# Performance work log

Hardware: AMD Instinct MI355X
Metric: run time of the kernel (lower is better)

Reference implementation:

```python
import jax, jax.numpy as jnp
import numpy as np

T, B, E, H = 64, 64, 128, 256
N_ITEMS, N_DATA = 50000, 20000
EPS = 1e-8


def setup_inputs() -> dict:
    key = jax.random.key(0)
    ks = jax.random.split(key, 20)
    lengths = jnp.sort(jax.random.randint(ks[0], (B,), 1, T + 1))[::-1]
    lengths = lengths.at[0].set(T)  # pack_padded_sequence expects max length first
    x = jax.random.randint(ks[1], (T, B), 1, N_ITEMS)
    tmask = jnp.arange(T)[:, None] < lengths[None, :]
    x = jnp.where(tmask, x, 0)  # padding index 0
    s = 0.05
    emb_table = (jax.random.normal(ks[2], (N_ITEMS, E)) * s).at[0].set(0.0)  # padding_idx=0
    data_embeddings = jax.random.normal(ks[3], (N_DATA, E)) * s
    return {
        'x': x, 'lengths': lengths,
        'emb_table': emb_table, 'data_embeddings': data_embeddings,
        'W_ih': jax.random.normal(ks[4], (4 * H, E)) * s,
        'W_hh': jax.random.normal(ks[5], (4 * H, H)) * s,
        'b_ih': jax.random.normal(ks[6], (4 * H,)) * s,
        'b_hh': jax.random.normal(ks[7], (4 * H,)) * s,
        'Wq': jax.random.normal(ks[8], (H, H)) * s, 'bq': jax.random.normal(ks[9], (H,)) * s,
        'Wk': jax.random.normal(ks[10], (H, H)) * s, 'bk': jax.random.normal(ks[11], (H,)) * s,
        'Wv': jax.random.normal(ks[12], (H, H)) * s, 'bv': jax.random.normal(ks[13], (H,)) * s,
        'W_out': jax.random.normal(ks[14], (E, H)) * s, 'b_out': jax.random.normal(ks[15], (E,)) * s,
    }


def _forward(x, lengths, emb_table, data_embeddings, W_ih, W_hh, b_ih, b_hh,
             Wq, bq, Wk, bk, Wv, bv, W_out, b_out):
    t_len, b_sz = x.shape
    e_dim = emb_table.shape[1]
    h_dim = W_hh.shape[1]

    embs0 = emb_table[x]  # (T, B, E); dropout is identity in eval mode
    initial_embs = jax.lax.stop_gradient(embs0)  # .clone().detach() in original

    # PositionalEncoding: original slices by x.size(1) == batch dim (faithful quirk)
    pos = jnp.arange(b_sz, dtype=jnp.float32)[:, None]
    div = jnp.exp(jnp.arange(0, e_dim, 2, dtype=jnp.float32) * (-jnp.log(10000.0) / e_dim))
    enc = jnp.stack([jnp.sin(pos * div), jnp.cos(pos * div)], axis=-1).reshape(b_sz, e_dim)
    embs = embs0 + enc[None, :, :]  # broadcast over time

    # single-layer LSTM over time (gate order i, f, g, o)
    def step(carry, x_t):
        h, c = carry
        gates = x_t @ W_ih.T + h @ W_hh.T + (b_ih + b_hh)  # (B, 4H)
        i, f, g, o = jnp.split(gates, 4, axis=-1)
        c = jax.nn.sigmoid(f) * c + jax.nn.sigmoid(i) * jnp.tanh(g)
        h = jax.nn.sigmoid(o) * jnp.tanh(c)
        return (h, c), h

    h0 = jnp.zeros((b_sz, h_dim), embs.dtype)
    (_, _), lstm_out = jax.lax.scan(step, (h0, h0), embs)  # (T, B, H)

    # pack/pad round-trip zeroes outputs past each length (LSTM is causal)
    tmask = jnp.arange(t_len)[:, None] < lengths[None, :]  # (T, B)
    lstm_out = lstm_out * tmask[:, :, None]
    lstm_out = lstm_out.transpose(1, 0, 2)  # (B, T, H)

    padding_mask = jnp.sum(lstm_out, axis=-1) != 0  # (B, T)

    q = lstm_out @ Wq.T + bq
    k = lstm_out @ Wk.T + bk
    v = lstm_out @ Wv.T + bv
    score = jnp.einsum('bth,bsh->bts', q, k) / jnp.sqrt(jnp.float32(h_dim))
    score = jnp.where(padding_mask[:, None, :], score, -jnp.inf)
    attn = jax.nn.softmax(score, axis=2)
    weighted = jnp.einsum('bts,bsh->bth', attn, v)  # (B, T, H)
    attn_output = jnp.mean(weighted, axis=1) @ W_out.T + b_out  # (B, E)

    # kNN: fused normalize + matmul + argmin + gather over all T at once
    qn = initial_embs / jnp.clip(jnp.linalg.norm(initial_embs, axis=-1, keepdims=True), EPS)
    dn = data_embeddings / jnp.clip(jnp.linalg.norm(data_embeddings, axis=-1, keepdims=True), EPS)
    sims = jnp.einsum('tbe,ne->tbn', qn, dn)  # (T, B, N_DATA)
    idx = jnp.argmax(sims, axis=-1)  # argmin of (1 - sim)
    closest = jnp.mean(data_embeddings[idx], axis=0)  # (B, E)

    attn_output = attn_output * closest
    return attn_output @ emb_table.T  # (B, n_items)


def reference(x, lengths, emb_table, data_embeddings, W_ih, W_hh, b_ih, b_hh,
              Wq, bq, Wk, bk, Wv, bv, W_out, b_out):
    return _forward(x, lengths, emb_table, data_embeddings, W_ih, W_hh, b_ih, b_hh,
                    Wq, bq, Wk, bk, Wv, bv, W_out, b_out)
```

## Files before the change

kernel.cpp:

```cpp
#include <hip/hip_runtime.h>

typedef unsigned int uint;
typedef unsigned short ushort;
typedef unsigned long long u64;

#define NITEMS 50000
#define NDATA  20000
#define BLKCAP 4096u
#define OVCAP  65536u

#define OFF_LSTMOUT   0x0000000ULL
#define OFF_HX        0x0400000ULL
#define OFF_PACKED    0x0440000ULL
#define OFF_PACKED2   0x0448000ULL
#define OFF_HITCNTS   0x0450000ULL
#define OFF_OHITCNT   0x0450800ULL
#define MEMSET_BYTES  0x0451000ULL
#define OFF_QMARGIN   0x0451000ULL
#define OFF_XW        0x0560000ULL
#define OFF_QKV       0x1560000ULL
#define OFF_HITBUF    OFF_QKV
#define OFF_WIHT      0x2160000ULL
#define OFF_WQKVT     0x21E0000ULL
#define OFF_BIASIH    0x22A0000ULL
#define OFF_BQKV      0x22A1000ULL
#define OFF_DNSCALE   0x22A2000ULL
#define OFF_CLOSEST   0x22B6000ULL
#define OFF_AV        0x22BE000ULL
#define OFF_DEMB16    0x22C6000ULL
#define OFF_A16       0x27A8000ULL

__device__ __forceinline__ ushort f2bf(float f) {
  union { float f; uint u; } v; v.f = f;
  uint u = v.u;
  return (ushort)((u + 0x7FFFu + ((u >> 16) & 1u)) >> 16);
}
__device__ __forceinline__ uint fkey(float f) {
  union { float f; uint u; } v; v.f = f;
  return (v.u & 0x80000000u) ? ~v.u : (v.u | 0x80000000u);
}
__device__ __forceinline__ u64 shfl_xor_u64(u64 v, int off) {
  uint lo = (uint)v, hi = (uint)(v >> 32);
  lo = (uint)__shfl_xor((int)lo, off);
  hi = (uint)__shfl_xor((int)hi, off);
  return ((u64)hi << 32) | (u64)lo;
}

typedef __attribute__((ext_vector_type(8))) short short8;
typedef __attribute__((ext_vector_type(4))) float floatx4;

#define R32(M) M(0) M(1) M(2) M(3) M(4) M(5) M(6) M(7) M(8) M(9) M(10) M(11) \
  M(12) M(13) M(14) M(15) M(16) M(17) M(18) M(19) M(20) M(21) M(22) M(23) \
  M(24) M(25) M(26) M(27) M(28) M(29) M(30) M(31)

__global__ __launch_bounds__(256) void prep_kernel(
    const int* __restrict__ x,
    const float* __restrict__ emb, const float* __restrict__ demb,
    const float* __restrict__ W_ih,
    const float* __restrict__ Wq, const float* __restrict__ Wk, const float* __restrict__ Wv,
    const float* __restrict__ b_ih, const float* __restrict__ b_hh,
    const float* __restrict__ bq, const float* __restrict__ bk, const float* __restrict__ bv,
    float* __restrict__ dnscale, ushort* __restrict__ demb16, ushort* __restrict__ a16,
    float* __restrict__ wiht, float* __restrict__ wqkvt,
    float* __restrict__ biasih, float* __restrict__ bqkv,
    float* __restrict__ qmargin, u64* __restrict__ packed2)
{
  int blk = blockIdx.x, tid = threadIdx.x;
  if (blk < 5000) {
    int row = blk * 4 + (tid >> 6);
    int lane = tid & 63;
    float2 d = *(const float2*)(demb + (size_t)row * 128 + lane * 2);
    float s = d.x * d.x + d.y * d.y;
    for (int off = 32; off; off >>= 1) s += __shfl_xor(s, off);
    if (lane == 0) dnscale[row] = 1.0f / fmaxf(sqrtf(s), 1e-8f);
  } else if (blk < 6250) {
    size_t base = ((size_t)(blk - 5000) * 256 + tid) * 8;
    float4 f1 = *(const float4*)(demb + base);
    float4 f2 = *(const float4*)(demb + base + 4);
    uint4 o;
    o.x = (uint)f2bf(f1.x) | ((uint)f2bf(f1.y) << 16);
    o.y = (uint)f2bf(f1.z) | ((uint)f2bf(f1.w) << 16);
    o.z = (uint)f2bf(f2.x) | ((uint)f2bf(f2.y) << 16);
    o.w = (uint)f2bf(f2.z) | ((uint)f2bf(f2.w) << 16);
    *(uint4*)(demb16 + base) = o;
  } else if (blk < 6506) {
    int idx = (blk - 6250) * 256 + tid;
    int m = idx >> 4, seg = idx & 15;
    const float* src = emb + (size_t)x[m] * 128 + seg * 8;
    float4 f1 = *(const float4*)(src);
    float4 f2 = *(const float4*)(src + 4);
    uint4 o;
    o.x = (uint)f2bf(f1.x) | ((uint)f2bf(f1.y) << 16);
    o.y = (uint)f2bf(f1.z) | ((uint)f2bf(f1.w) << 16);
    o.z = (uint)f2bf(f2.x) | ((uint)f2bf(f2.y) << 16);
    o.w = (uint)f2bf(f2.z) | ((uint)f2bf(f2.w) << 16);
    *(uint4*)(a16 + (size_t)m * 128 + seg * 8) = o;
  } else if (blk < 7018) {
    int f = (blk - 6506) * 256 + tid;
    int r = f >> 7, e = f & 127;
    wiht[e * 1024 + r] = W_ih[f];
  } else if (blk < 7786) {
    int f = (blk - 7018) * 256 + tid;
    int w = f >> 16; int rem = f & 65535;
    int r = rem >> 8, e = rem & 255;
    const float* src = (w == 0) ? Wq : (w == 1) ? Wk : Wv;
    wqkvt[e * 768 + w * 256 + r] = src[rem];
  } else if (blk < 7790) {
    int idx = (blk - 7786) * 256 + tid;
    if (idx < 1024) biasih[idx] = b_ih[idx] + b_hh[idx];
  } else if (blk < 7793) {
    int idx = (blk - 7790) * 256 + tid;
    if (idx < 768) {
      int w = idx >> 8; int r = idx & 255;
      const float* src = (w == 0) ? bq : (w == 1) ? bk : bv;
      bqkv[idx] = src[r];
    }
  } else {
    int row = (blk - 7793) * 4 + (tid >> 6);
    int lane = tid & 63;
    float2 d = *(const float2*)(emb + (size_t)x[row] * 128 + lane * 2);
    float s = d.x * d.x + d.y * d.y;
    for (int off = 32; off; off >>= 1) s += __shfl_xor(s, off);
    if (lane == 0) {
      if (s == 0.f) {
        qmargin[row] = -1e30f;
        packed2[row] = ((u64)fkey(0.0f) << 32) | 0xFFFFFFFFull;
      } else {
        qmargin[row] = 0.017f * sqrtf(s) + 1e-5f;
      }
    }
  }
}

__global__ __launch_bounds__(256) void xw_kernel(
    const int* __restrict__ x, const float* __restrict__ emb,
    const float* __restrict__ wiht, const float* __restrict__ biasih,
    float* __restrict__ xW)
{
  __shared__ __align__(16) float At[128 * 16];
  int blk = blockIdx.x, tid = threadIdx.x;
  int m0 = blk * 16;
  for (int c = 0; c < 8; ++c) {
    int idx = c * 256 + tid;
    int mm = idx >> 7, e = idx & 127;
    int m = m0 + mm;
    int bcol = m & 63;
    int xv = x[m];
    float val = emb[(size_t)xv * 128 + e];
    int j = e >> 1;
    float arg = (float)bcol * __expf((float)j * -0.14391157f);
    val += (e & 1) ? cosf(arg) : sinf(arg);
    At[e * 16 + mm] = val;
  }
  __syncthreads();
  int quad = tid >> 6, l = tid & 63;
  for (int rp = 0; rp < 4; ++rp) {
    int r = rp * 256 + l * 4;
    float acc[4][4] = {};
    for (int e = 0; e < 128; ++e) {
      float4 wv4 = *(const float4*)(wiht + e * 1024 + r);
      float4 av4 = *(const float4*)(At + e * 16 + quad * 4);
      float am[4] = {av4.x, av4.y, av4.z, av4.w};
      float wr4[4] = {wv4.x, wv4.y, wv4.z, wv4.w};
      #pragma unroll
      for (int mi = 0; mi < 4; ++mi)
        #pragma unroll
        for (int ri = 0; ri < 4; ++ri)
          acc[mi][ri] += am[mi] * wr4[ri];
    }
    float4 bv4 = *(const float4*)(biasih + r);
    #pragma unroll
    for (int mi = 0; mi < 4; ++mi) {
      size_t m = (size_t)(m0 + quad * 4 + mi);
      float4 o;
      o.x = acc[mi][0] + bv4.x; o.y = acc[mi][1] + bv4.y;
      o.z = acc[mi][2] + bv4.z; o.w = acc[mi][3] + bv4.w;
      *(float4*)(xW + m * 1024 + r) = o;
    }
  }
}

__global__ __launch_bounds__(256) void knn_kernel(
    const ushort* __restrict__ a16, const ushort* __restrict__ demb16,
    const float* __restrict__ dnscale, const float* __restrict__ qmargin,
    u64* __restrict__ packed, uint* __restrict__ hitcnts, uint* __restrict__ ohitcnt,
    uint* __restrict__ hitbuf)
{
  __shared__ __align__(16) ushort b_sh[2][64 * 144];
  __shared__ uint lcnt;
  int blk = blockIdx.x, tid = threadIdx.x;
  int chunk = blk & 15, mt = blk >> 4;
  int wv = tid >> 6, lane = tid & 63;
  int col = lane & 15, quad = lane >> 4;
  int M0 = mt * 128;
  if (tid == 0) lcnt = 0;
  short8 afrag[2][4];
  #pragma unroll
  for (int s = 0; s < 2; ++s) {
    int mrow = M0 + s * 64 + wv * 16 + col;
    #pragma unroll
    for (int kf = 0; kf < 4; ++kf)
      afrag[s][kf] = *(const short8*)(a16 + (size_t)mrow * 128 + kf * 32 + quad * 8);
  }
  float best[2][4] = {{-1e30f,-1e30f,-1e30f,-1e30f},{-1e30f,-1e30f,-1e30f,-1e30f}};
  int bidx[2][4] = {};
  int nbase = chunk * 1250, nend = nbase + 1250;
  const int niter = 20;
  int srow = tid >> 4, sseg = tid & 15;
  uint4 stg[4]; float scr[4];

  #pragma unroll
  for (int p = 0; p < 4; ++p) {
    int n = nbase + p * 16 + srow;
    uint4 v = {0u,0u,0u,0u};
    if (n < nend) v = *(const uint4*)(demb16 + (size_t)n * 128 + sseg * 8);
    stg[p] = v;
  }
  #pragma unroll
  for (int ns = 0; ns < 4; ++ns) {
    int n = nbase + ns * 16 + col;
    scr[ns] = (n < nend) ? dnscale[n] : 0.f;
  }
  for (int it = 0; it < niter; ++it) {
    int n0 = nbase + it * 64;
    ushort* bsh = b_sh[it & 1];
    #pragma unroll
    for (int p = 0; p < 4; ++p)
      *(uint4*)(&bsh[(p * 16 + srow) * 144 + sseg * 8]) = stg[p];
    float mysc[4] = {scr[0], scr[1], scr[2], scr[3]};
    __syncthreads();
    if (it + 1 < niter) {
      int nb = n0 + 64;
      #pragma unroll
      for (int p = 0; p < 4; ++p) {
        int n = nb + p * 16 + srow;
        uint4 v = {0u,0u,0u,0u};
        if (n < nend) v = *(const uint4*)(demb16 + (size_t)n * 128 + sseg * 8);
        stg[p] = v;
      }
      #pragma unroll
      for (int ns = 0; ns < 4; ++ns) {
        int n = nb + ns * 16 + col;
        scr[ns] = (n < nend) ? dnscale[n] : 0.f;
      }
    }
    #pragma unroll
    for (int ns = 0; ns < 4; ++ns) {
      short8 bfr[4];
      #pragma unroll
      for (int kf = 0; kf < 4; ++kf)
        bfr[kf] = *(const short8*)(&bsh[(ns * 16 + col) * 144 + kf * 32 + quad * 8]);
      int n = n0 + ns * 16 + col;
      float sc = mysc[ns];
      bool valid = (n < nend);
      #pragma unroll
      for (int s = 0; s < 2; ++s) {
        floatx4 acc = {0.f, 0.f, 0.f, 0.f};
        #pragma unroll
        for (int kf = 0; kf < 4; ++kf)
          acc = __builtin_amdgcn_mfma_f32_16x16x32_bf16(afrag[s][kf], bfr[kf], acc, 0, 0, 0);
        #pragma unroll
        for (int r = 0; r < 4; ++r) {
          float sim = acc[r] * sc;
          if (valid && sim > best[s][r]) { best[s][r] = sim; bidx[s][r] = n; }
        }
      }
    }
  }
  float thr[2][4];
  #pragma unroll
  for (int s = 0; s < 2; ++s)
    #pragma unroll
    for (int r = 0; r < 4; ++r) {
      u64 p = ((u64)fkey(best[s][r]) << 32) | (u64)(0xFFFFFFFFu - (uint)bidx[s][r]);
      #pragma unroll
      for (int off = 1; off < 16; off <<= 1) {
        u64 o = shfl_xor_u64(p, off);
        if (o > p) p = o;
      }
      int m = M0 + s * 64 + wv * 16 + quad * 4 + r;
      union { uint u; float f; } bu;
      uint k = (uint)(p >> 32);
      bu.u = (k & 0x80000000u) ? (k & 0x7FFFFFFFu) : ~k;
      thr[s][r] = bu.f - qmargin[m];
      if (col == 0)
        atomicMax((unsigned long long*)&packed[m], (unsigned long long)p);
    }
  __syncthreads();

  uint* myregion = hitbuf + (size_t)blk * BLKCAP;
  uint* ovregion = hitbuf + (size_t)512 * BLKCAP;
  #pragma unroll
  for (int p = 0; p < 4; ++p) {
    int n = nbase + p * 16 + srow;
    uint4 v = {0u,0u,0u,0u};
    if (n < nend) v = *(const uint4*)(demb16 + (size_t)n * 128 + sseg * 8);
    stg[p] = v;
  }
  #pragma unroll
  for (int ns = 0; ns < 4; ++ns) {
    int n = nbase + ns * 16 + col;
    scr[ns] = (n < nend) ? dnscale[n] : 0.f;
  }
  for (int it = 0; it < niter; ++it) {
    int n0 = nbase + it * 64;
    ushort* bsh = b_sh[it & 1];
    #pragma unroll
    for (int p = 0; p < 4; ++p)
      *(uint4*)(&bsh[(p * 16 + srow) * 144 + sseg * 8]) = stg[p];
    float mysc[4] = {scr[0], scr[1], scr[2], scr[3]};
    __syncthreads();
    if (it + 1 < niter) {
      int nb = n0 + 64;
      #pragma unroll
      for (int p = 0; p < 4; ++p) {
        int n = nb + p * 16 + srow;
        uint4 v = {0u,0u,0u,0u};
        if (n < nend) v = *(const uint4*)(demb16 + (size_t)n * 128 + sseg * 8);
        stg[p] = v;
      }
      #pragma unroll
      for (int ns = 0; ns < 4; ++ns) {
        int n = nb + ns * 16 + col;
        scr[ns] = (n < nend) ? dnscale[n] : 0.f;
      }
    }
    #pragma unroll
    for (int ns = 0; ns < 4; ++ns) {
      short8 bfr[4];
      #pragma unroll
      for (int kf = 0; kf < 4; ++kf)
        bfr[kf] = *(const short8*)(&bsh[(ns * 16 + col) * 144 + kf * 32 + quad * 8]);
      int n = n0 + ns * 16 + col;
      float sc = mysc[ns];
      bool valid = (n < nend);
      #pragma unroll
      for (int s = 0; s < 2; ++s) {
        floatx4 acc = {0.f, 0.f, 0.f, 0.f};
        #pragma unroll
        for (int kf = 0; kf < 4; ++kf)
          acc = __builtin_amdgcn_mfma_f32_16x16x32_bf16(afrag[s][kf], bfr[kf], acc, 0, 0, 0);
        #pragma unroll
        for (int r = 0; r < 4; ++r) {
          float sim = acc[r] * sc;
          bool hit = valid && (sim >= thr[s][r]);
          u64 mask = __ballot(hit);
          if (mask) {
            uint lcntv = (uint)__popcll(mask);
            int leader = __ffsll((unsigned long long)mask) - 1;
            uint base = 0;
            if (lane == leader) base = atomicAdd(&lcnt, lcntv);
            base = (uint)__shfl((int)base, leader);
            if (hit) {
              uint pos = base + (uint)__popcll(mask & ((1ull << lane) - 1ull));
              uint mm = (uint)(M0 + s * 64 + wv * 16 + quad * 4 + r);
              uint rec = (mm << 15) | (uint)n;
              if (pos < BLKCAP) {
                myregion[pos] = rec;
              } else {
                uint op = atomicAdd(ohitcnt, 1u);
                if (op < OVCAP) ovregion[op] = rec;
              }
            }
          }
        }
      }
    }
  }
  __syncthreads();
  if (tid == 0) hitcnts[blk] = lcnt;
}

__global__ __launch_bounds__(256) void rescore_kernel(
    const uint* __restrict__ hitbuf, const uint* __restrict__ hitcnts,
    const uint* __restrict__ ohitcnt, const u64* __restrict__ packed,
    const int* __restrict__ x, const float* __restrict__ emb,
    const float* __restrict__ demb, const float* __restrict__ dnscale,
    u64* __restrict__ packed2)
{
  int blk = blockIdx.x, tid = threadIdx.x;
  uint gid = blk * 256 + tid;
  if (gid < 4096) {
    uint m = gid;
    uint n = 0xFFFFFFFFu - (uint)(packed[m] & 0xFFFFFFFFull);
    if (n < NDATA) {
      const float* q = emb + (size_t)x[m] * 128;
      const float* d = demb + (size_t)n * 128;
      double p = 0.0;
      #pragma unroll 8
      for (int e = 0; e < 128; e += 2) {
        float2 qv = *(const float2*)(q + e);
        float2 dv = *(const float2*)(d + e);
        p += (double)qv.x * (double)dv.x + (double)qv.y * (double)dv.y;
      }
      float sx = (float)(p * (double)dnscale[n]);
      u64 key = ((u64)fkey(sx) << 32) | (u64)(0xFFFFFFFFu - n);
      atomicMax((unsigned long long*)&packed2[m], (unsigned long long)key);
    }
  }
  const uint* src; uint cnt; uint stride;
  if (blk < 512) {
    src = hitbuf + (size_t)blk * BLKCAP;
    cnt = hitcnts[blk]; if (cnt > BLKCAP) cnt = BLKCAP;
    stride = 256;
  } else {
    src = hitbuf + (size_t)512 * BLKCAP + (blk - 512) * 256 + 0;
    src = hitbuf + (size_t)512 * BLKCAP;
    cnt = *ohitcnt; if (cnt > OVCAP) cnt = OVCAP;
    stride = 16 * 256;
  }
  uint start = (blk < 512) ? tid : (uint)((blk - 512) * 256 + tid);
  for (uint h = start; h < cnt; h += stride) {
    uint rec = src[h];
    uint m = rec >> 15, n = rec & 0x7FFFu;
    if (m >= 4096 || n >= NDATA) continue;
    const float* q = emb + (size_t)x[m] * 128;
    const float* d = demb + (size_t)n * 128;
    double p = 0.0;
    #pragma unroll 8
    for (int e = 0; e < 128; e += 2) {
      float2 qv = *(const float2*)(q + e);
      float2 dv = *(const float2*)(d + e);
      p += (double)qv.x * (double)dv.x + (double)qv.y * (double)dv.y;
    }
    float sx = (float)(p * (double)dnscale[n]);
    u64 key = ((u64)fkey(sx) << 32) | (u64)(0xFFFFFFFFu - n);
    atomicMax((unsigned long long*)&packed2[m], (unsigned long long)key);
  }
}

__global__ __launch_bounds__(512, 2) void lstm_kernel(
    const int* __restrict__ lengths, const float* __restrict__ Whh,
    const float* __restrict__ xW, float* __restrict__ lstm_out,
    u64* __restrict__ hx)
{
  __shared__ __align__(16) float h_sh[256];
  __shared__ float part_sh[512];
  int blk = blockIdx.x, tid = threadIdx.x;
  int b = blk & 63, q = blk >> 6;
  int row_local = tid >> 1, half = tid & 1;
  int gate = row_local >> 6, jloc = row_local & 63;
  int grow = gate * 256 + q * 64 + jloc;
  const float4* wp4 = (const float4*)(Whh + (size_t)grow * 256 + half * 128);
#define WDECL(i) float4 tt##i = wp4[i]; \
  float w##i##x = tt##i.x, w##i##y = tt##i.y, w##i##z = tt##i.z, w##i##w = tt##i.w;
  R32(WDECL)
#define WPIN(i) asm volatile("" : "+v"(w##i##x), "+v"(w##i##y), "+v"(w##i##z), "+v"(w##i##w));
  R32(WPIN)
  int len = lengths[b];
  if (tid < 256) h_sh[tid] = 0.f;
  float cval = 0.f;
  int jr = (tid < q * 64) ? tid : tid + 64;
  __syncthreads();
  for (int t = 0; t < len; ++t) {
    if (t > 0) {
      if (tid < 192) {
        u64* slot = hx + (((size_t)(t & 1) * 64 + b) * 256 + jr);
        u64 v = 0; int guard = 0;
        while (true) {
          v = __hip_atomic_load(slot, __ATOMIC_RELAXED, __HIP_MEMORY_SCOPE_AGENT);
          if ((uint)v == (uint)t || ++guard > (1 << 22)) break;
          __builtin_amdgcn_s_sleep(1);
        }
        union { uint u; float f; } cv; cv.u = (uint)(v >> 32);
        h_sh[jr] = cv.f;
      }
      __syncthreads();
    }
    const float4* h4 = (const float4*)(h_sh + half * 128);
    float acc = 0.f;
#define WACC(i) { float4 hv = h4[i]; \
    acc += w##i##x * hv.x + w##i##y * hv.y + w##i##z * hv.z + w##i##w * hv.w; }
    R32(WACC)
    part_sh[tid] = acc;
    __syncthreads();
    if (tid < 64) {
      const float* xwrow = xW + ((size_t)t * 64 + b) * 1024 + q * 64 + tid;
      float gi = part_sh[tid * 2]         + part_sh[tid * 2 + 1]         + xwrow[0];
      float gf = part_sh[(64 + tid) * 2]  + part_sh[(64 + tid) * 2 + 1]  + xwrow[256];
      float gg = part_sh[(128 + tid) * 2] + part_sh[(128 + tid) * 2 + 1] + xwrow[512];
      float go = part_sh[(192 + tid) * 2] + part_sh[(192 + tid) * 2 + 1] + xwrow[768];
      float ii = 1.f / (1.f + __expf(-gi));
      float ff = 1.f / (1.f + __expf(-gf));
      float oo = 1.f / (1.f + __expf(-go));
      cval = ff * cval + ii * tanhf(gg);
      float hv = oo * tanhf(cval);
      int j = q * 64 + tid;
      lstm_out[((size_t)b * 64 + t) * 256 + j] = hv;
      h_sh[j] = hv;
      union { float f; uint u; } cu; cu.f = hv;
      u64 pk = ((u64)cu.u << 32) | (u64)(uint)(t + 1);
      __hip_atomic_store(hx + (((size_t)((t + 1) & 1) * 64 + b) * 256 + j), pk,
                         __ATOMIC_RELAXED, __HIP_MEMORY_SCOPE_AGENT);
    }
    __syncthreads();
  }
}

__global__ __launch_bounds__(128) void closest_kernel(
    const u64* __restrict__ packed2, const float* __restrict__ demb,
    float* __restrict__ closest)
{
  int b = blockIdx.x, tid = threadIdx.x;
  float s = 0.f;
  for (int t = 0; t < 64; ++t) {
    uint low = (uint)(packed2[t * 64 + b] & 0xFFFFFFFFull);
    uint n = 0xFFFFFFFFu - low;
    if (n >= NDATA) n = 0;
    s += demb[(size_t)n * 128 + tid];
  }
  closest[b * 128 + tid] = s * (1.0f / 64.0f);
}

__global__ __launch_bounds__(256) void qkv_kernel(
    const float* __restrict__ lstm_out, const float* __restrict__ wqkvt,
    const float* __restrict__ bqkv, float* __restrict__ qkv)
{
  __shared__ __align__(16) float At[256 * 16];
  int blk = blockIdx.x, tid = threadIdx.x;
  int m0 = blk * 16;
  for (int c = 0; c < 16; ++c)
    At[tid * 16 + c] = lstm_out[((size_t)m0 + c) * 256 + tid];
  __syncthreads();
  int quad = tid >> 6, l = tid & 63;
  for (int rp = 0; rp < 3; ++rp) {
    int r = rp * 256 + l * 4;
    float acc[4][4] = {};
    for (int e = 0; e < 256; ++e) {
      float4 wv4 = *(const float4*)(wqkvt + (size_t)e * 768 + r);
      float4 av4 = *(const float4*)(At + e * 16 + quad * 4);
      float am[4] = {av4.x, av4.y, av4.z, av4.w};
      float wr4[4] = {wv4.x, wv4.y, wv4.z, wv4.w};
      #pragma unroll
      for (int mi = 0; mi < 4; ++mi)
        #pragma unroll
        for (int ri = 0; ri < 4; ++ri)
          acc[mi][ri] += am[mi] * wr4[ri];
    }
    float4 bv4 = *(const float4*)(bqkv + r);
    #pragma unroll
    for (int mi = 0; mi < 4; ++mi) {
      size_t m = (size_t)(m0 + quad * 4 + mi);
      float4 o;
      o.x = acc[mi][0] + bv4.x; o.y = acc[mi][1] + bv4.y;
      o.z = acc[mi][2] + bv4.z; o.w = acc[mi][3] + bv4.w;
      *(float4*)(qkv + m * 768 + r) = o;
    }
  }
}

__global__ __launch_bounds__(256) void attn_kernel(
    const float* __restrict__ qkv, const int* __restrict__ lengths,
    const float* __restrict__ closest, const float* __restrict__ W_out,
    const float* __restrict__ b_out, float* __restrict__ av)
{
  __shared__ float k_sh[64 * 257];
  __shared__ __align__(16) float q_sh[4 * 256];
  __shared__ float wpart[4 * 64];
  __shared__ float wtot[64];
  __shared__ float out_sh[256];
  int b = blockIdx.x, tid = threadIdx.x;
  int wv = tid >> 6, lane = tid & 63;
  int len = lengths[b];
  for (int s = 0; s < 64; ++s)
    k_sh[s * 257 + tid] = qkv[((size_t)b * 64 + s) * 768 + 256 + tid];
  wpart[tid] = 0.f;
  for (int tq = 0; tq < 16; ++tq) {
    __syncthreads();
    #pragma unroll
    for (int c = 0; c < 4; ++c)
      q_sh[c * 256 + tid] = qkv[((size_t)b * 64 + tq * 4 + c) * 768 + tid];
    __syncthreads();
    const float* krow = k_sh + lane * 257;
    const float* qrow = q_sh + wv * 256;
    float sc = 0.f;
    #pragma unroll 8
    for (int h = 0; h < 256; ++h)
      sc += qrow[h] * krow[h];
    sc *= 0.0625f;
    bool vs = (lane < len);
    float scm = vs ? sc : -1e30f;
    float mx = scm;
    for (int off = 32; off; off >>= 1) mx = fmaxf(mx, __shfl_xor(mx, off));
    float e = vs ? __expf(sc - mx) : 0.f;
    float sum = e;
    for (int off = 32; off; off >>= 1) sum += __shfl_xor(sum, off);
    wpart[wv * 64 + lane] += e / sum;
  }
  __syncthreads();
  if (tid < 64)
    wtot[tid] = (wpart[tid] + wpart[64 + tid] + wpart[128 + tid] + wpart[192 + tid]) * (1.0f / 64.0f);
  __syncthreads();
  {
    float acc = 0.f;
    for (int s = 0; s < 64; ++s)
      acc += wtot[s] * qkv[((size_t)b * 64 + s) * 768 + 512 + tid];
    out_sh[tid] = acc;
  }
  __syncthreads();
  if (tid < 128) {
    const float4* wr = (const float4*)(W_out + (size_t)tid * 256);
    float p = b_out[tid];
    #pragma unroll
    for (int c = 0; c < 64; ++c) {
      float4 u = wr[c];
      p += out_sh[c * 4 + 0] * u.x + out_sh[c * 4 + 1] * u.y
         + out_sh[c * 4 + 2] * u.z + out_sh[c * 4 + 3] * u.w;
    }
    av[tid * 64 + b] = p * closest[b * 128 + tid];
  }
}

__global__ __launch_bounds__(256) void final_kernel(
    const float* __restrict__ emb, const float* __restrict__ av,
    float* __restrict__ out)
{
  int i = blockIdx.x * 256 + threadIdx.x;
  if (i >= NITEMS) return;
  const float4* row = (const float4*)(emb + (size_t)i * 128);
  float acc[64];
  #pragma unroll
  for (int bb = 0; bb < 64; ++bb) acc[bb] = 0.f;
  for (int e4 = 0; e4 < 32; ++e4) {
    float4 u = row[e4];
    float wvv[4] = {u.x, u.y, u.z, u.w};
    const float* ab = av + e4 * 4 * 64;
    #pragma unroll
    for (int j = 0; j < 4; ++j) {
      #pragma unroll
      for (int bb = 0; bb < 64; ++bb)
        acc[bb] += wvv[j] * ab[j * 64 + bb];
    }
  }
  #pragma unroll
  for (int bb = 0; bb < 64; ++bb)
    out[(size_t)bb * NITEMS + i] = acc[bb];
}

extern "C" void kernel_launch(void* const* d_in, const int* in_sizes, int n_in,
                              void* d_out, int out_size, void* d_ws, size_t ws_size,
                              hipStream_t stream)
{
  const int*   x       = (const int*)d_in[0];
  const int*   lengths = (const int*)d_in[1];
  const float* emb     = (const float*)d_in[2];
  const float* demb    = (const float*)d_in[3];
  const float* W_ih    = (const float*)d_in[4];
  const float* W_hh    = (const float*)d_in[5];
  const float* b_ih    = (const float*)d_in[6];
  const float* b_hh    = (const float*)d_in[7];
  const float* Wq      = (const float*)d_in[8];
  const float* bq      = (const float*)d_in[9];
  const float* Wk      = (const float*)d_in[10];
  const float* bk      = (const float*)d_in[11];
  const float* Wv      = (const float*)d_in[12];
  const float* bv      = (const float*)d_in[13];
  const float* W_out   = (const float*)d_in[14];
  const float* b_out   = (const float*)d_in[15];

  char* ws = (char*)d_ws;
  float*  lstm_out = (float*)(ws + OFF_LSTMOUT);
  u64*    hx       = (u64*)(ws + OFF_HX);
  u64*    packed   = (u64*)(ws + OFF_PACKED);
  u64*    packed2  = (u64*)(ws + OFF_PACKED2);
  uint*   hitcnts  = (uint*)(ws + OFF_HITCNTS);
  uint*   ohitcnt  = (uint*)(ws + OFF_OHITCNT);
  float*  qmargin  = (float*)(ws + OFF_QMARGIN);
  uint*   hitbuf   = (uint*)(ws + OFF_HITBUF);
  float*  xW       = (float*)(ws + OFF_XW);
  float*  qkv      = (float*)(ws + OFF_QKV);
  float*  wiht     = (float*)(ws + OFF_WIHT);
  float*  wqkvt    = (float*)(ws + OFF_WQKVT);
  float*  biasih   = (float*)(ws + OFF_BIASIH);
  float*  bqkv     = (float*)(ws + OFF_BQKV);
  float*  dnscale  = (float*)(ws + OFF_DNSCALE);
  float*  closest  = (float*)(ws + OFF_CLOSEST);
  float*  av       = (float*)(ws + OFF_AV);
  ushort* demb16   = (ushort*)(ws + OFF_DEMB16);
  ushort* a16      = (ushort*)(ws + OFF_A16);

  hipMemsetAsync(d_ws, 0, (size_t)MEMSET_BYTES, stream);

  hipLaunchKernelGGL(prep_kernel, dim3(8817), dim3(256), 0, stream,
                     x, emb, demb, W_ih, Wq, Wk, Wv, b_ih, b_hh, bq, bk, bv,
                     dnscale, demb16, a16, wiht, wqkvt, biasih, bqkv,
                     qmargin, packed2);
  hipLaunchKernelGGL(xw_kernel, dim3(256), dim3(256), 0, stream,
                     x, emb, wiht, biasih, xW);
  hipLaunchKernelGGL(knn_kernel, dim3(512), dim3(256), 0, stream,
                     a16, demb16, dnscale, qmargin, packed, hitcnts, ohitcnt, hitbuf);
  hipLaunchKernelGGL(rescore_kernel, dim3(528), dim3(256), 0, stream,
                     hitbuf, hitcnts, ohitcnt, packed, x, emb, demb, dnscale, packed2);
  hipLaunchKernelGGL(lstm_kernel, dim3(256), dim3(512), 0, stream,
                     lengths, W_hh, xW, lstm_out, hx);
  hipLaunchKernelGGL(closest_kernel, dim3(64), dim3(128), 0, stream,
                     packed2, demb, closest);
  hipLaunchKernelGGL(qkv_kernel, dim3(256), dim3(256), 0, stream,
                     lstm_out, wqkvt, bqkv, qkv);
  hipLaunchKernelGGL(attn_kernel, dim3(64), dim3(256), 0, stream,
                     qkv, lengths, closest, W_out, b_out, av);
  hipLaunchKernelGGL(final_kernel, dim3(196), dim3(256), 0, stream,
                     emb, av, (float*)d_out);
}
```

Before: 616.3 us.

## Store W_hh as bf16 in LDS for LSTM and widen kNN M-tile

The LSTM kernel now reads its W_hh slice from a bf16 copy made in the prep kernel and keeps it in padded shared memory instead of 128 pinned VGPRs, which frees registers and lets more waves or blocks run. The kNN kernel processes 256 query rows per block over smaller data chunks (32 chunks of 625), reusing each staged data tile across twice as many queries. The rescore start-index logic is tidied. Converting W_hh to bf16 reduces recurrent precision, and the larger kNN tile raises register pressure.

```diff
diff --git a/kernel.cpp b/kernel.cpp
--- a/kernel.cpp
+++ b/kernel.cpp
@@ -29,7 +29,14 @@
 #define OFF_AV        0x22BE000ULL
 #define OFF_DEMB16    0x22C6000ULL
 #define OFF_A16       0x27A8000ULL
-
+#define OFF_WHH16     0x28A8000ULL
+
+__device__ __forceinline__ float bflo(uint u) {
+  union { uint i; float f; } v; v.i = u << 16; return v.f;
+}
+__device__ __forceinline__ float bfhi(uint u) {
+  union { uint i; float f; } v; v.i = u & 0xFFFF0000u; return v.f;
+}
 __device__ __forceinline__ ushort f2bf(float f) {
   union { float f; uint u; } v; v.f = f;
   uint u = v.u;
@@ -49,18 +56,15 @@
 typedef __attribute__((ext_vector_type(8))) short short8;
 typedef __attribute__((ext_vector_type(4))) float floatx4;
 
-#define R32(M) M(0) M(1) M(2) M(3) M(4) M(5) M(6) M(7) M(8) M(9) M(10) M(11) \
-  M(12) M(13) M(14) M(15) M(16) M(17) M(18) M(19) M(20) M(21) M(22) M(23) \
-  M(24) M(25) M(26) M(27) M(28) M(29) M(30) M(31)
-
 __global__ __launch_bounds__(256) void prep_kernel(
     const int* __restrict__ x,
     const float* __restrict__ emb, const float* __restrict__ demb,
-    const float* __restrict__ W_ih,
+    const float* __restrict__ W_ih, const float* __restrict__ W_hh,
     const float* __restrict__ Wq, const float* __restrict__ Wk, const float* __restrict__ Wv,
     const float* __restrict__ b_ih, const float* __restrict__ b_hh,
     const float* __restrict__ bq, const float* __restrict__ bk, const float* __restrict__ bv,
     float* __restrict__ dnscale, ushort* __restrict__ demb16, ushort* __restrict__ a16,
+    ushort* __restrict__ whh16,
     float* __restrict__ wiht, float* __restrict__ wqkvt,
     float* __restrict__ biasih, float* __restrict__ bqkv,
     float* __restrict__ qmargin, u64* __restrict__ packed2)
@@ -115,8 +119,18 @@
       const float* src = (w == 0) ? bq : (w == 1) ? bk : bv;
       bqkv[idx] = src[r];
     }
+  } else if (blk < 7921) {
+    size_t base = ((size_t)(blk - 7793) * 256 + tid) * 8;
+    float4 f1 = *(const float4*)(W_hh + base);
+    float4 f2 = *(const float4*)(W_hh + base + 4);
+    uint4 o;
+    o.x = (uint)f2bf(f1.x) | ((uint)f2bf(f1.y) << 16);
+    o.y = (uint)f2bf(f1.z) | ((uint)f2bf(f1.w) << 16);
+    o.z = (uint)f2bf(f2.x) | ((uint)f2bf(f2.y) << 16);
+    o.w = (uint)f2bf(f2.z) | ((uint)f2bf(f2.w) << 16);
+    *(uint4*)(whh16 + base) = o;
   } else {
-    int row = (blk - 7793) * 4 + (tid >> 6);
+    int row = (blk - 7921) * 4 + (tid >> 6);
     int lane = tid & 63;
     float2 d = *(const float2*)(emb + (size_t)x[row] * 128 + lane * 2);
     float s = d.x * d.x + d.y * d.y;
@@ -189,23 +203,27 @@
   __shared__ __align__(16) ushort b_sh[2][64 * 144];
   __shared__ uint lcnt;
   int blk = blockIdx.x, tid = threadIdx.x;
-  int chunk = blk & 15, mt = blk >> 4;
+  int chunk = blk & 31, mt = blk >> 5;
   int wv = tid >> 6, lane = tid & 63;
   int col = lane & 15, quad = lane >> 4;
-  int M0 = mt * 128;
+  int M0 = mt * 256;
   if (tid == 0) lcnt = 0;
-  short8 afrag[2][4];
-  #pragma unroll
-  for (int s = 0; s < 2; ++s) {
+  short8 afrag[4][4];
+  #pragma unroll
+  for (int s = 0; s < 4; ++s) {
     int mrow = M0 + s * 64 + wv * 16 + col;
     #pragma unroll
     for (int kf = 0; kf < 4; ++kf)
       afrag[s][kf] = *(const short8*)(a16 + (size_t)mrow * 128 + kf * 32 + quad * 8);
   }
-  float best[2][4] = {{-1e30f,-1e30f,-1e30f,-1e30f},{-1e30f,-1e30f,-1e30f,-1e30f}};
-  int bidx[2][4] = {};
-  int nbase = chunk * 1250, nend = nbase + 1250;
-  const int niter = 20;
+  float best[4][4];
+  int bidx[4][4] = {};
+  #pragma unroll
+  for (int s = 0; s < 4; ++s)
+    #pragma unroll
+    for (int r = 0; r < 4; ++r) best[s][r] = -1e30f;
+  int nbase = chunk * 625, nend = nbase + 625;
+  const int niter = 10;
   int srow = tid >> 4, sseg = tid & 15;
   uint4 stg[4]; float scr[4];
 
@@ -254,7 +272,7 @@
       float sc = mysc[ns];
       bool valid = (n < nend);
       #pragma unroll
-      for (int s = 0; s < 2; ++s) {
+      for (int s = 0; s < 4; ++s) {
         floatx4 acc = {0.f, 0.f, 0.f, 0.f};
         #pragma unroll
         for (int kf = 0; kf < 4; ++kf)
@@ -267,9 +285,9 @@
       }
     }
   }
-  float thr[2][4];
-  #pragma unroll
-  for (int s = 0; s < 2; ++s)
+  float thr[4][4];
+  #pragma unroll
+  for (int s = 0; s < 4; ++s)
     #pragma unroll
     for (int r = 0; r < 4; ++r) {
       u64 p = ((u64)fkey(best[s][r]) << 32) | (u64)(0xFFFFFFFFu - (uint)bidx[s][r]);
@@ -335,7 +353,7 @@
       float sc = mysc[ns];
       bool valid = (n < nend);
       #pragma unroll
-      for (int s = 0; s < 2; ++s) {
+      for (int s = 0; s < 4; ++s) {
         floatx4 acc = {0.f, 0.f, 0.f, 0.f};
         #pragma unroll
         for (int kf = 0; kf < 4; ++kf)
@@ -398,18 +416,16 @@
       atomicMax((unsigned long long*)&packed2[m], (unsigned long long)key);
     }
   }
-  const uint* src; uint cnt; uint stride;
+  const uint* src; uint cnt; uint stride; uint start;
   if (blk < 512) {
     src = hitbuf + (size_t)blk * BLKCAP;
     cnt = hitcnts[blk]; if (cnt > BLKCAP) cnt = BLKCAP;
-    stride = 256;
+    stride = 256; start = tid;
   } else {
-    src = hitbuf + (size_t)512 * BLKCAP + (blk - 512) * 256 + 0;
     src = hitbuf + (size_t)512 * BLKCAP;
     cnt = *ohitcnt; if (cnt > OVCAP) cnt = OVCAP;
-    stride = 16 * 256;
-  }
-  uint start = (blk < 512) ? tid : (uint)((blk - 512) * 256 + tid);
+    stride = 16 * 256; start = (uint)((blk - 512) * 256 + tid);
+  }
   for (uint h = start; h < cnt; h += stride) {
     uint rec = src[h];
     uint m = rec >> 15, n = rec & 0x7FFFu;
@@ -429,24 +445,26 @@
   }
 }
 
-__global__ __launch_bounds__(512, 2) void lstm_kernel(
-    const int* __restrict__ lengths, const float* __restrict__ Whh,
+__global__ __launch_bounds__(512) void lstm_kernel(
+    const int* __restrict__ lengths, const ushort* __restrict__ whh16,
     const float* __restrict__ xW, float* __restrict__ lstm_out,
     u64* __restrict__ hx)
 {
+  extern __shared__ ushort wlds[];
   __shared__ __align__(16) float h_sh[256];
   __shared__ float part_sh[512];
   int blk = blockIdx.x, tid = threadIdx.x;
   int b = blk & 63, q = blk >> 6;
-  int row_local = tid >> 1, half = tid & 1;
-  int gate = row_local >> 6, jloc = row_local & 63;
+  int lr = tid >> 1, half = tid & 1;
+  int gate = lr >> 6, jloc = lr & 63;
   int grow = gate * 256 + q * 64 + jloc;
-  const float4* wp4 = (const float4*)(Whh + (size_t)grow * 256 + half * 128);
-#define WDECL(i) float4 tt##i = wp4[i]; \
-  float w##i##x = tt##i.x, w##i##y = tt##i.y, w##i##z = tt##i.z, w##i##w = tt##i.w;
-  R32(WDECL)
-#define WPIN(i) asm volatile("" : "+v"(w##i##x), "+v"(w##i##y), "+v"(w##i##z), "+v"(w##i##w));
-  R32(WPIN)
+  {
+    const uint2* src = (const uint2*)(whh16 + (size_t)grow * 256 + half * 128);
+    ushort* dst = wlds + lr * 260 + half * 128;
+    #pragma unroll
+    for (int c = 0; c < 32; ++c)
+      *(uint2*)(dst + c * 4) = src[c];
+  }
   int len = lengths[b];
   if (tid < 256) h_sh[tid] = 0.f;
   float cval = 0.f;
@@ -468,10 +486,15 @@
       __syncthreads();
     }
     const float4* h4 = (const float4*)(h_sh + half * 128);
+    const uint2* wrow = (const uint2*)(wlds + lr * 260 + half * 128);
     float acc = 0.f;
-#define WACC(i) { float4 hv = h4[i]; \
-    acc += w##i##x * hv.x + w##i##y * hv.y + w##i##z * hv.z + w##i##w * hv.w; }
-    R32(WACC)
+    #pragma unroll
+    for (int c = 0; c < 32; ++c) {
+      uint2 wv = wrow[c];
+      float4 hv = h4[c];
+      acc += bflo(wv.x) * hv.x + bfhi(wv.x) * hv.y
+           + bflo(wv.y) * hv.z + bfhi(wv.y) * hv.w;
+    }
     part_sh[tid] = acc;
     __syncthreads();
     if (tid < 64) {
@@ -678,12 +701,13 @@
   float*  av       = (float*)(ws + OFF_AV);
   ushort* demb16   = (ushort*)(ws + OFF_DEMB16);
   ushort* a16      = (ushort*)(ws + OFF_A16);
+  ushort* whh16    = (ushort*)(ws + OFF_WHH16);
 
   hipMemsetAsync(d_ws, 0, (size_t)MEMSET_BYTES, stream);
 
-  hipLaunchKernelGGL(prep_kernel, dim3(8817), dim3(256), 0, stream,
-                     x, emb, demb, W_ih, Wq, Wk, Wv, b_ih, b_hh, bq, bk, bv,
-                     dnscale, demb16, a16, wiht, wqkvt, biasih, bqkv,
+  hipLaunchKernelGGL(prep_kernel, dim3(8945), dim3(256), 0, stream,
+                     x, emb, demb, W_ih, W_hh, Wq, Wk, Wv, b_ih, b_hh, bq, bk, bv,
+                     dnscale, demb16, a16, whh16, wiht, wqkvt, biasih, bqkv,
                      qmargin, packed2);
   hipLaunchKernelGGL(xw_kernel, dim3(256), dim3(256), 0, stream,
                      x, emb, wiht, biasih, xW);
@@ -691,8 +715,8 @@
                      a16, demb16, dnscale, qmargin, packed, hitcnts, ohitcnt, hitbuf);
   hipLaunchKernelGGL(rescore_kernel, dim3(528), dim3(256), 0, stream,
                      hitbuf, hitcnts, ohitcnt, packed, x, emb, demb, dnscale, packed2);
-  hipLaunchKernelGGL(lstm_kernel, dim3(256), dim3(512), 0, stream,
-                     lengths, W_hh, xW, lstm_out, hx);
+  hipLaunchKernelGGL(lstm_kernel, dim3(256), dim3(512), 256 * 260 * 2, stream,
+                     lengths, whh16, xW, lstm_out, hx);
   hipLaunchKernelGGL(closest_kernel, dim3(64), dim3(128), 0, stream,
                      packed2, demb, closest);
   hipLaunchKernelGGL(qkv_kernel, dim3(256), dim3(256), 0, stream,
```

New measurement: 672.4 us. +9.1%, slower.
